# Kernel tuning notes

Measured on AMD Instinct MI355X. Metric: run time of the kernel, lower is better.

Reference implementation:

```python
import jax, jax.numpy as jnp
import numpy as np

HS = 768      # hidden_size
NH = 12       # num_heads
HD = HS // NH # head_dim = 64
WS = 8        # window_size
NG = 4        # num_global_tokens
EPS = 1e-6


def _rmsnorm(x, w):
    return x * jax.lax.rsqrt(jnp.mean(x * x, axis=-1, keepdims=True) + EPS) * w


def _attn(q, k, v, scale):
    s = jnp.einsum('...qd,...kd->...qk', q, k) * scale
    return jnp.einsum('...qk,...kd->...qd', jax.nn.softmax(s, axis=-1), v)


def _heads(t):
    # (B*, S, D) -> (B*, H, S, hd)
    return t.reshape(t.shape[0], t.shape[1], NH, HD).transpose(0, 2, 1, 3)


def setup_inputs() -> dict:
    key = jax.random.key(0)
    k0, k1, k2, k3 = jax.random.split(key, 4)
    B, N = 8, 4096
    x = jax.random.normal(k0, (B, N, HS), dtype=jnp.float32)
    w_qkv = jax.random.normal(k1, (HS, 3 * HS), dtype=jnp.float32) * 0.02
    w_out = jax.random.normal(k2, (HS, HS), dtype=jnp.float32) * 0.02
    q_norm_w = jnp.ones((HD,), dtype=jnp.float32)
    k_norm_w = jnp.ones((HD,), dtype=jnp.float32)
    global_tokens = jax.random.normal(k3, (1, NG, HS), dtype=jnp.float32) * 0.02
    return {'x': x, 'w_qkv': w_qkv, 'w_out': w_out,
            'q_norm_w': q_norm_w, 'k_norm_w': k_norm_w,
            'global_tokens': global_tokens}


def reference(x, w_qkv, w_out, q_norm_w, k_norm_w, global_tokens):
    B, N, D = x.shape
    h = w = int(np.sqrt(N))
    ws = WS
    scale = HD ** -0.5
    # ---- window partition (B, N, D) -> (B*nW, ws*ws, D) ----
    pad_h = (ws - h % ws) % ws
    pad_w = (ws - w % ws) % ws
    xg = x.reshape(B, h, w, D)
    if pad_h or pad_w:
        xg = jnp.pad(xg, ((0, 0), (0, pad_h), (0, pad_w), (0, 0)))
    hp, wp = h + pad_h, w + pad_w
    xl = xg.reshape(B, hp // ws, ws, wp // ws, ws, D)
    xl = xl.transpose(0, 1, 3, 2, 4, 5).reshape(-1, ws * ws, D)
    # ---- local window attention ----
    q, k, v = jnp.split(xl @ w_qkv, 3, axis=-1)
    q, k, v = _heads(q), _heads(k), _heads(v)
    q = _rmsnorm(q, q_norm_w)
    k = _rmsnorm(k, k_norm_w)
    o = _attn(q, k, v, scale)                      # (B*nW, H, ws*ws, hd)
    o = o.transpose(0, 2, 1, 3).reshape(-1, ws * ws, D)
    # ---- window unpartition ----
    o = o.reshape(B, hp // ws, wp // ws, ws, ws, D)
    o = o.transpose(0, 1, 3, 2, 4, 5).reshape(B, hp, wp, D)[:, :h, :w].reshape(B, N, D)
    # ---- global register tokens attend over [global; all tokens] ----
    g = jnp.broadcast_to(global_tokens, (B, NG, D))
    xf = jnp.concatenate([g, x], axis=1)           # (B, NG+N, D)
    qg, kg, vg = jnp.split(xf @ w_qkv, 3, axis=-1)
    qg = _heads(qg[:, :NG])                        # (B, H, NG, hd) -- no qk_norm in global path
    ka, va = _heads(kg), _heads(vg)                # (B, H, NG+N, hd)
    og = _attn(qg, ka, va, scale).transpose(0, 2, 1, 3).reshape(B, NG, D)
    o = o + og.mean(axis=1, keepdims=True)
    return o @ w_out
```

## Files before the change

### kernel.cpp

```cpp
#include <hip/hip_runtime.h>
#include <hip/hip_bf16.h>

typedef short short8 __attribute__((ext_vector_type(8)));
typedef unsigned short ushort8 __attribute__((ext_vector_type(8)));
typedef unsigned short ushort4v __attribute__((ext_vector_type(4)));
typedef float f32x4 __attribute__((ext_vector_type(4)));
typedef unsigned short ushort;

constexpr float SCALE = 0.125f;
constexpr float EPS_RMS = 1e-6f;

#define BAR() asm volatile("s_barrier" ::: "memory")
#define WAITV(N) asm volatile("s_waitcnt vmcnt(" #N ")" ::: "memory")

__device__ __forceinline__ ushort f2bf(float f) {
  return __builtin_bit_cast(unsigned short, __float2bfloat16(f));
}
__device__ __forceinline__ float bf2f(ushort u) {
  return __bfloat162float(__builtin_bit_cast(__hip_bfloat16, u));
}
__device__ __forceinline__ void gl_lds16(const void* g, void* l) {
  __builtin_amdgcn_global_load_lds((const __attribute__((address_space(1))) void*)g,
                                   (__attribute__((address_space(3))) void*)l, 16, 0, 0);
}

__device__ __forceinline__ int nat_row(int p) {
  return (p & ~4095) | (((p >> 9) & 7) << 9) | (((p >> 3) & 7) << 6) |
         (((p >> 6) & 7) << 3) | (p & 7);
}

__global__ void k_prep(const float* __restrict__ src, int src_ld, int mode,
                       ushort* __restrict__ hi, ushort* __restrict__ lo) {
  __shared__ float tile[64][65];
  int rb = blockIdx.x, db = blockIdx.y;
  int tid = threadIdx.x;
#pragma unroll
  for (int e = 0; e < 16; ++e) {
    int idx = e * 256 + tid;
    int dd = idx >> 6, cc = idx & 63;
    int sc;
    if (mode == 0) { int h = rb / 3, p = rb % 3; sc = p * 768 + h * 64 + cc; }
    else sc = rb * 64 + cc;
    tile[dd][cc] = src[(db * 64 + dd) * src_ld + sc];
  }
  __syncthreads();
#pragma unroll
  for (int e = 0; e < 16; ++e) {
    int idx = e * 256 + tid;
    int cc = idx >> 6, dd = idx & 63;
    float f = tile[dd][cc];
    ushort h = f2bf(f);
    ushort l = f2bf(f - bf2f(h));
    int o = (rb * 64 + cc) * 768 + db * 64 + dd;
    hi[o] = h;
    lo[o] = l;
  }
}

__global__ void k_xsplit(const float* __restrict__ x,
                         ushort* __restrict__ xh, ushort* __restrict__ xl) {
  int idx = blockIdx.x * 256 + threadIdx.x;
  int p = idx / 96, seg = idx - p * 96;
  int n = nat_row(p);
  const float* src = x + n * 768 + seg * 8;
  float4 a = *(const float4*)src;
  float4 c = *(const float4*)(src + 4);
  float v[8] = {a.x, a.y, a.z, a.w, c.x, c.y, c.z, c.w};
  ushort8 hi, lo;
#pragma unroll
  for (int j = 0; j < 8; ++j) {
    ushort h = f2bf(v[j]);
    hi[j] = h;
    lo[j] = f2bf(v[j] - bf2f(h));
  }
  *(ushort8*)&xh[p * 768 + seg * 8] = hi;
  *(ushort8*)&xl[p * 768 + seg * 8] = lo;
}

__global__ void k_gqkv(const float* __restrict__ gtok,
                       const float* __restrict__ w_qkv,
                       float* __restrict__ qkv_g) {
  int idx = blockIdx.x * 256 + threadIdx.x;
  int tok = idx / 2304, c = idx - tok * 2304;
  const float* gp = gtok + tok * 768;
  float s = 0.f;
  for (int d = 0; d < 768; ++d) s += gp[d] * w_qkv[d * 2304 + c];
  qkv_g[idx] = s;
}

#define QS_OFF 0
#define KT_OFF 4352
#define VS_OFF 8704
#define SQ_OFF 13056
#define SK_OFF 13120
#define PC_OFF 13248

__global__ __launch_bounds__(256, 2) void k_fused(
    const ushort* __restrict__ xh, const ushort* __restrict__ xl,
    const ushort* __restrict__ Whi, const ushort* __restrict__ Wlo,
    const float* __restrict__ qnw, const float* __restrict__ knw,
    const float* __restrict__ qkv_g, float* __restrict__ part,
    ushort* __restrict__ o_hi, ushort* __restrict__ o_lo) {
  __shared__ __align__(16) char smem[81920];
  const int tid = threadIdx.x;
  const int lane = tid & 63;
  const int wv = tid >> 6;
  const int wm = wv >> 1, wn = wv & 1;
  const int l15 = lane & 15, kq = lane >> 4;
  const int bid = blockIdx.x;
  const int xcd = bid & 7, kk_ = bid >> 3;
  const int h = kk_ % 12;
  const int mblk = (kk_ / 12) * 8 + xcd;
  const int r0 = mblk * 128;
  const int cb0 = h * 192;

  int gAo[4], lA[4]; bool pA[4];
#pragma unroll
  for (int j = 0; j < 4; ++j) {
    int byo = (j * 256 + tid) * 16;
    pA[j] = byo >= 8192;
    int wb = byo & 8191;
    int row = wb >> 6, sl = (wb >> 4) & 3;
    int kb = sl ^ ((row >> 1) & 3);
    gAo[j] = (r0 + row) * 768 + kb * 8;
    lA[j] = byo;
  }
  int gBo[6], lB[6]; bool pB[6];
#pragma unroll
  for (int j = 0; j < 6; ++j) {
    int byo = (j * 256 + tid) * 16;
    pB[j] = byo >= 12288;
    int wb = pB[j] ? byo - 12288 : byo;
    int row = wb >> 6, sl = (wb >> 4) & 3;
    int kb = sl ^ ((row >> 1) & 3);
    gBo[j] = (cb0 + row) * 768 + kb * 8;
    lB[j] = 16384 + byo;
  }

  f32x4 acc[4][6];
#pragma unroll
  for (int i = 0; i < 4; ++i)
#pragma unroll
    for (int j = 0; j < 6; ++j) acc[i][j] = (f32x4){0.f, 0.f, 0.f, 0.f};

  auto STAGE = [&](int t, int bufi) {
    const int kk = t * 32;
    char* bb = smem + bufi * 40960;
#pragma unroll
    for (int j = 0; j < 4; ++j) {
      const ushort* Ap = pA[j] ? xl : xh;
      gl_lds16(Ap + gAo[j] + kk, bb + lA[j]);
    }
#pragma unroll
    for (int j = 0; j < 6; ++j) {
      const ushort* Bp = pB[j] ? Wlo : Whi;
      gl_lds16(Bp + gBo[j] + kk, bb + lB[j]);
    }
  };

  auto COMPUTE = [&](int bufi) {
    const char* ba = smem + bufi * 40960;
    short8 ah[4], al[4], bh[6], bl[6];
#pragma unroll
    for (int mf = 0; mf < 4; ++mf) {
      int row = wm * 64 + mf * 16 + l15;
      int so = (kq ^ ((row >> 1) & 3)) << 4;
      ah[mf] = *(const short8*)(ba + row * 64 + so);
      al[mf] = *(const short8*)(ba + 8192 + row * 64 + so);
    }
#pragma unroll
    for (int nf = 0; nf < 6; ++nf) {
      int row = wn * 96 + nf * 16 + l15;
      int so = (kq ^ ((row >> 1) & 3)) << 4;
      bh[nf] = *(const short8*)(ba + 16384 + row * 64 + so);
      bl[nf] = *(const short8*)(ba + 28672 + row * 64 + so);
    }
#pragma unroll
    for (int mf = 0; mf < 4; ++mf)
#pragma unroll
      for (int nf = 0; nf < 6; ++nf) {
        acc[mf][nf] = __builtin_amdgcn_mfma_f32_16x16x32_bf16(ah[mf], bh[nf], acc[mf][nf], 0, 0, 0);
        acc[mf][nf] = __builtin_amdgcn_mfma_f32_16x16x32_bf16(ah[mf], bl[nf], acc[mf][nf], 0, 0, 0);
        acc[mf][nf] = __builtin_amdgcn_mfma_f32_16x16x32_bf16(al[mf], bh[nf], acc[mf][nf], 0, 0, 0);
      }
  };

  STAGE(0, 0); STAGE(1, 1);
  WAITV(10); BAR();
  for (int t = 0; t < 24; ++t) {
    int cur = t & 1;
    COMPUTE(cur);
    BAR();
    if (t < 22) { STAGE(t + 2, cur); WAITV(10); }
    else { WAITV(0); }
    BAR();
  }

  const int tl = tid;
  float* gb = (float*)smem;
  for (int pass = 0; pass < 2; ++pass) {
    if (wm == pass) {
#pragma unroll
      for (int mf = 0; mf < 4; ++mf) {
#pragma unroll
        for (int nf = 0; nf < 6; ++nf) {
          int col = wn * 96 + nf * 16 + l15;
#pragma unroll
          for (int e = 0; e < 4; ++e) {
            int tok = mf * 16 + kq * 4 + e;
            float val = acc[mf][nf][e];
            if (col < 64)       gb[QS_OFF + tok * 68 + col] = val;
            else if (col < 128) gb[KT_OFF + (col - 64) * 68 + tok] = val;
            else                gb[VS_OFF + tok * 68 + (col - 128)] = val;
          }
        }
      }
    }
    __syncthreads();

    const int widx = mblk * 2 + pass;
    const int b = widx >> 6, wl = widx & 63;

    {
      int qi = tl >> 6, j = tl & 63;
      const float* qgp = qkv_g + qi * 2304 + h * 64;
      float s = 0.f;
#pragma unroll 16
      for (int d = 0; d < 64; ++d) s += qgp[d] * gb[KT_OFF + d * 68 + j];
      s *= SCALE;
      float m = s;
#pragma unroll
      for (int o = 1; o < 64; o <<= 1) m = fmaxf(m, __shfl_xor(m, o));
      float p = expf(s - m);
      float l = p;
#pragma unroll
      for (int o = 1; o < 64; o <<= 1) l += __shfl_xor(l, o);
      gb[PC_OFF + qi * 64 + j] = p;
      int pbase = ((b * 12 + h) * 64 + wl) * 272;
      if (j == 0) { part[pbase + 256 + qi] = m; part[pbase + 260 + qi] = l; }
      __syncthreads();
      float a = 0.f;
#pragma unroll 16
      for (int jj = 0; jj < 64; ++jj) a += gb[PC_OFF + qi * 64 + jj] * gb[VS_OFF + jj * 68 + j];
      part[pbase + qi * 64 + j] = a;
    }
    __syncthreads();

    if (tl < 64) {
      float ss = 0.f;
#pragma unroll
      for (int d4 = 0; d4 < 16; ++d4) {
        f32x4 v = *(const f32x4*)&gb[QS_OFF + tl * 68 + d4 * 4];
        ss += v[0] * v[0] + v[1] * v[1] + v[2] * v[2] + v[3] * v[3];
      }
      gb[SQ_OFF + tl] = 1.0f / sqrtf(ss * 0.015625f + EPS_RMS);
    } else if (tl < 128) {
      int c = tl - 64;
      float ss = 0.f;
#pragma unroll 16
      for (int d = 0; d < 64; ++d) { float t = gb[KT_OFF + d * 68 + c]; ss += t * t; }
      gb[SK_OFF + c] = 1.0f / sqrtf(ss * 0.015625f + EPS_RMS);
    }
    __syncthreads();

    {
      const int ty = tl >> 4, tx = tl & 15;
      const int r0q = ty * 4, c0k = tx * 4;
      const f32x4* qnw4 = (const f32x4*)qnw;
      const f32x4* knw4 = (const f32x4*)knw;
      const f32x4 skv = *(const f32x4*)&gb[SK_OFF + c0k];
      f32x4 X[4];
      X[0] = X[1] = X[2] = X[3] = (f32x4){0.f, 0.f, 0.f, 0.f};
#pragma unroll
      for (int d4 = 0; d4 < 16; ++d4) {
        f32x4 ww = qnw4[d4] * knw4[d4];
        f32x4 k0 = *(const f32x4*)&gb[KT_OFF + (d4 * 4 + 0) * 68 + c0k];
        f32x4 k1 = *(const f32x4*)&gb[KT_OFF + (d4 * 4 + 1) * 68 + c0k];
        f32x4 k2 = *(const f32x4*)&gb[KT_OFF + (d4 * 4 + 2) * 68 + c0k];
        f32x4 k3 = *(const f32x4*)&gb[KT_OFF + (d4 * 4 + 3) * 68 + c0k];
#pragma unroll
        for (int r = 0; r < 4; ++r) {
          f32x4 qv = *(const f32x4*)&gb[QS_OFF + (r0q + r) * 68 + d4 * 4];
          qv *= ww;
          X[r] += qv[0] * k0 + qv[1] * k1 + qv[2] * k2 + qv[3] * k3;
        }
      }
      float li[4];
#pragma unroll
      for (int r = 0; r < 4; ++r) {
        X[r] = X[r] * skv * (gb[SQ_OFF + r0q + r] * SCALE);
        float m = fmaxf(fmaxf(X[r][0], X[r][1]), fmaxf(X[r][2], X[r][3]));
#pragma unroll
        for (int o = 1; o < 16; o <<= 1) m = fmaxf(m, __shfl_xor(m, o));
#pragma unroll
        for (int cc = 0; cc < 4; ++cc) X[r][cc] = expf(X[r][cc] - m);
        float s = X[r][0] + X[r][1] + X[r][2] + X[r][3];
#pragma unroll
        for (int o = 1; o < 16; o <<= 1) s += __shfl_xor(s, o);
        li[r] = 1.0f / s;
      }
      __syncthreads();
#pragma unroll
      for (int r = 0; r < 4; ++r)
        *(f32x4*)&gb[QS_OFF + (r0q + r) * 68 + c0k] = X[r];
      __syncthreads();
      f32x4 O[4];
      O[0] = O[1] = O[2] = O[3] = (f32x4){0.f, 0.f, 0.f, 0.f};
#pragma unroll
      for (int j4 = 0; j4 < 16; ++j4) {
        f32x4 v0 = *(const f32x4*)&gb[VS_OFF + (j4 * 4 + 0) * 68 + c0k];
        f32x4 v1 = *(const f32x4*)&gb[VS_OFF + (j4 * 4 + 1) * 68 + c0k];
        f32x4 v2 = *(const f32x4*)&gb[VS_OFF + (j4 * 4 + 2) * 68 + c0k];
        f32x4 v3 = *(const f32x4*)&gb[VS_OFF + (j4 * 4 + 3) * 68 + c0k];
#pragma unroll
        for (int r = 0; r < 4; ++r) {
          f32x4 pv = *(const f32x4*)&gb[QS_OFF + (r0q + r) * 68 + j4 * 4];
          O[r] += pv[0] * v0 + pv[1] * v1 + pv[2] * v2 + pv[3] * v3;
        }
      }
#pragma unroll
      for (int r = 0; r < 4; ++r) {
        O[r] *= li[r];
        int orow = (widx * 64 + r0q + r) * 768 + h * 64 + c0k;
        ushort4v hv, lv;
#pragma unroll
        for (int cc = 0; cc < 4; ++cc) {
          float a = O[r][cc];
          ushort hh = f2bf(a);
          hv[cc] = hh;
          lv[cc] = f2bf(a - bf2f(hh));
        }
        *(ushort4v*)&o_hi[orow] = hv;
        *(ushort4v*)&o_lo[orow] = lv;
      }
    }
    __syncthreads();
  }
}

__global__ __launch_bounds__(256, 2) void k_proj8(
    const ushort* __restrict__ o_hi, const ushort* __restrict__ o_lo,
    const ushort* __restrict__ Whi, const ushort* __restrict__ Wlo,
    const float* __restrict__ g_term, float* __restrict__ out) {
  __shared__ __align__(16) char smem[81920];
  const int tid = threadIdx.x;
  const int lane = tid & 63;
  const int wv = tid >> 6;
  const int wm = wv >> 1, wn = wv & 1;
  const int l15 = lane & 15, kq = lane >> 4;
  const int bid = blockIdx.x;
  const int xcd = bid & 7, kk_ = bid >> 3;
  const int cblk = kk_ % 4;
  const int mblk = (kk_ / 4) * 8 + xcd;
  const int r0 = mblk * 128;
  const int cb0 = cblk * 192;

  int gAo[4], lA[4]; bool pA[4];
#pragma unroll
  for (int j = 0; j < 4; ++j) {
    int byo = (j * 256 + tid) * 16;
    pA[j] = byo >= 8192;
    int wb = byo & 8191;
    int row = wb >> 6, sl = (wb >> 4) & 3;
    int kb = sl ^ ((row >> 1) & 3);
    gAo[j] = (r0 + row) * 768 + kb * 8;
    lA[j] = byo;
  }
  int gBo[6], lB[6]; bool pB[6];
#pragma unroll
  for (int j = 0; j < 6; ++j) {
    int byo = (j * 256 + tid) * 16;
    pB[j] = byo >= 12288;
    int wb = pB[j] ? byo - 12288 : byo;
    int row = wb >> 6, sl = (wb >> 4) & 3;
    int kb = sl ^ ((row >> 1) & 3);
    gBo[j] = (cb0 + row) * 768 + kb * 8;
    lB[j] = 16384 + byo;
  }

  f32x4 acc[4][6];
#pragma unroll
  for (int i = 0; i < 4; ++i)
#pragma unroll
    for (int j = 0; j < 6; ++j) acc[i][j] = (f32x4){0.f, 0.f, 0.f, 0.f};

  auto STAGE = [&](int t, int bufi) {
    const int kk = t * 32;
    char* bb = smem + bufi * 40960;
#pragma unroll
    for (int j = 0; j < 4; ++j) {
      const ushort* Ap = pA[j] ? o_lo : o_hi;
      gl_lds16(Ap + gAo[j] + kk, bb + lA[j]);
    }
#pragma unroll
    for (int j = 0; j < 6; ++j) {
      const ushort* Bp = pB[j] ? Wlo : Whi;
      gl_lds16(Bp + gBo[j] + kk, bb + lB[j]);
    }
  };

  auto COMPUTE = [&](int bufi) {
    const char* ba = smem + bufi * 40960;
    short8 ah[4], al[4], bh[6], bl[6];
#pragma unroll
    for (int mf = 0; mf < 4; ++mf) {
      int row = wm * 64 + mf * 16 + l15;
      int so = (kq ^ ((row >> 1) & 3)) << 4;
      ah[mf] = *(const short8*)(ba + row * 64 + so);
      al[mf] = *(const short8*)(ba + 8192 + row * 64 + so);
    }
#pragma unroll
    for (int nf = 0; nf < 6; ++nf) {
      int row = wn * 96 + nf * 16 + l15;
      int so = (kq ^ ((row >> 1) & 3)) << 4;
      bh[nf] = *(const short8*)(ba + 16384 + row * 64 + so);
      bl[nf] = *(const short8*)(ba + 28672 + row * 64 + so);
    }
#pragma unroll
    for (int mf = 0; mf < 4; ++mf)
#pragma unroll
      for (int nf = 0; nf < 6; ++nf) {
        acc[mf][nf] = __builtin_amdgcn_mfma_f32_16x16x32_bf16(ah[mf], bh[nf], acc[mf][nf], 0, 0, 0);
        acc[mf][nf] = __builtin_amdgcn_mfma_f32_16x16x32_bf16(ah[mf], bl[nf], acc[mf][nf], 0, 0, 0);
        acc[mf][nf] = __builtin_amdgcn_mfma_f32_16x16x32_bf16(al[mf], bh[nf], acc[mf][nf], 0, 0, 0);
      }
  };

  STAGE(0, 0); STAGE(1, 1);
  WAITV(10); BAR();
  for (int t = 0; t < 24; ++t) {
    int cur = t & 1;
    COMPUTE(cur);
    BAR();
    if (t < 22) { STAGE(t + 2, cur); WAITV(10); }
    else { WAITV(0); }
    BAR();
  }

#pragma unroll
  for (int mf = 0; mf < 4; ++mf) {
    int prow0 = r0 + wm * 64 + mf * 16 + kq * 4;
#pragma unroll
    for (int nf = 0; nf < 6; ++nf) {
      int col = cb0 + wn * 96 + nf * 16 + l15;
#pragma unroll
      for (int e = 0; e < 4; ++e) {
        int p = prow0 + e;
        out[nat_row(p) * 768 + col] = acc[mf][nf][e] + g_term[(p >> 12) * 768 + col];
      }
    }
  }
}

__global__ void k_greduce(const float* __restrict__ qkv_g,
                          const float* __restrict__ part,
                          float* __restrict__ og_mean) {
  __shared__ float red[4][64];
  int bh = blockIdx.x;
  int b = bh / 12, h = bh - b * 12;
  int tid = threadIdx.x;
  int qi = tid >> 6, d = tid & 63;
  float M = -1e30f, L = 0.f, A = 0.f;
  float qd = qkv_g[qi * 2304 + h * 64 + d];
#pragma unroll
  for (int gk = 0; gk < 4; ++gk) {
    float kd = qkv_g[gk * 2304 + 768 + h * 64 + d];
    float prod = qd * kd;
#pragma unroll
    for (int o = 1; o < 64; o <<= 1) prod += __shfl_xor(prod, o);
    float s = prod * SCALE;
    float Mn = fmaxf(M, s);
    float f = expf(M - Mn), e = expf(s - Mn);
    float vd = qkv_g[gk * 2304 + 1536 + h * 64 + d];
    A = A * f + e * vd;
    L = L * f + e;
    M = Mn;
  }
  for (int p = 0; p < 64; ++p) {
    int pbase = ((b * 12 + h) * 64 + p) * 272;
    float mp = part[pbase + 256 + qi];
    float lp = part[pbase + 260 + qi];
    float ap = part[pbase + qi * 64 + d];
    float Mn = fmaxf(M, mp);
    float f = expf(M - Mn), e = expf(mp - Mn);
    A = A * f + ap * e;
    L = L * f + lp * e;
    M = Mn;
  }
  red[qi][d] = A / L;
  __syncthreads();
  if (tid < 64) {
    float s = (red[0][d] + red[1][d] + red[2][d] + red[3][d]) * 0.25f;
    og_mean[b * 768 + h * 64 + d] = s;
  }
}

__global__ void k_gterm(const float* __restrict__ og_mean,
                        const float* __restrict__ w_out,
                        float* __restrict__ g_term) {
  int idx = blockIdx.x * 256 + threadIdx.x;
  int b = idx / 768, c = idx - b * 768;
  const float* op = og_mean + b * 768;
  float s = 0.f;
  for (int d = 0; d < 768; ++d) s += op[d] * w_out[d * 768 + c];
  g_term[idx] = s;
}

extern "C" void kernel_launch(void* const* d_in, const int* in_sizes, int n_in,
                              void* d_out, int out_size, void* d_ws, size_t ws_size,
                              hipStream_t stream) {
  const float* x      = (const float*)d_in[0];
  const float* w_qkv  = (const float*)d_in[1];
  const float* w_out  = (const float*)d_in[2];
  const float* qnw    = (const float*)d_in[3];
  const float* knw    = (const float*)d_in[4];
  const float* gtok   = (const float*)d_in[5];
  float* out = (float*)d_out;

  ushort* WhiQ = (ushort*)d_ws;
  ushort* WloQ = WhiQ + 2304 * 768;
  ushort* WhiO = WloQ + 2304 * 768;
  ushort* WloO = WhiO + 768 * 768;
  ushort* o_hi = WloO + 768 * 768;
  ushort* o_lo = o_hi + 32768 * 768;
  float* qkv_g   = (float*)(o_lo + 32768 * 768);
  float* part    = qkv_g + 9216;
  float* og_mean = part + 8 * 12 * 64 * 272;
  float* g_term  = og_mean + 6144;

  ushort* xh = (ushort*)d_out;
  ushort* xl = xh + 32768 * 768;

  k_prep  <<<dim3(36, 12), 256, 0, stream>>>(w_qkv, 2304, 0, WhiQ, WloQ);
  k_prep  <<<dim3(12, 12), 256, 0, stream>>>(w_out,  768, 1, WhiO, WloO);
  k_gqkv  <<<36,    256, 0, stream>>>(gtok, w_qkv, qkv_g);
  k_xsplit<<<12288, 256, 0, stream>>>(x, xh, xl);

  k_fused <<<3072, 256, 0, stream>>>(xh, xl, WhiQ, WloQ, qnw, knw, qkv_g, part, o_hi, o_lo);

  k_greduce<<<96, 256, 0, stream>>>(qkv_g, part, og_mean);
  k_gterm  <<<24, 256, 0, stream>>>(og_mean, w_out, g_term);
  k_proj8 <<<1024, 256, 0, stream>>>(o_hi, o_lo, WhiO, WloO, g_term, out);
}
```

Measured before the change: 690.1 us.

## Halve fused kernel M-tile to one window per block, drop two-pass epilogue

Each k_fused block now handles one 64-token window instead of two (64x192 tile, 6144 blocks). This halves LDS to 64KB and the accumulator registers, so more blocks can be resident and the serial two-pass epilogue goes away. Some syncthreads are removed, the global-attention PV step is merged into the RMS phase, and qnw*knw is precomputed in LDS. It also adds s_setprio around the MFMA loops and uses fast __expf. The cost is that the W tile is reloaded twice as often per token, which adds global and L2 traffic.

```diff
diff --git a/kernel.cpp b/kernel.cpp
--- a/kernel.cpp
+++ b/kernel.cpp
@@ -94,6 +94,7 @@
 #define SQ_OFF 13056
 #define SK_OFF 13120
 #define PC_OFF 13248
+#define WW_OFF 13504
 
 __global__ __launch_bounds__(256, 2) void k_fused(
     const ushort* __restrict__ xh, const ushort* __restrict__ xl,
@@ -101,7 +102,7 @@
     const float* __restrict__ qnw, const float* __restrict__ knw,
     const float* __restrict__ qkv_g, float* __restrict__ part,
     ushort* __restrict__ o_hi, ushort* __restrict__ o_lo) {
-  __shared__ __align__(16) char smem[81920];
+  __shared__ __align__(16) char smem[65536];
   const int tid = threadIdx.x;
   const int lane = tid & 63;
   const int wv = tid >> 6;
@@ -111,15 +112,15 @@
   const int xcd = bid & 7, kk_ = bid >> 3;
   const int h = kk_ % 12;
   const int mblk = (kk_ / 12) * 8 + xcd;
-  const int r0 = mblk * 128;
+  const int r0 = mblk * 64;
   const int cb0 = h * 192;
 
-  int gAo[4], lA[4]; bool pA[4];
-#pragma unroll
-  for (int j = 0; j < 4; ++j) {
+  int gAo[2], lA[2]; bool pA[2];
+#pragma unroll
+  for (int j = 0; j < 2; ++j) {
     int byo = (j * 256 + tid) * 16;
-    pA[j] = byo >= 8192;
-    int wb = byo & 8191;
+    pA[j] = byo >= 4096;
+    int wb = byo & 4095;
     int row = wb >> 6, sl = (wb >> 4) & 3;
     int kb = sl ^ ((row >> 1) & 3);
     gAo[j] = (r0 + row) * 768 + kb * 8;
@@ -134,20 +135,20 @@
     int row = wb >> 6, sl = (wb >> 4) & 3;
     int kb = sl ^ ((row >> 1) & 3);
     gBo[j] = (cb0 + row) * 768 + kb * 8;
-    lB[j] = 16384 + byo;
-  }
-
-  f32x4 acc[4][6];
-#pragma unroll
-  for (int i = 0; i < 4; ++i)
+    lB[j] = 8192 + byo;
+  }
+
+  f32x4 acc[2][6];
+#pragma unroll
+  for (int i = 0; i < 2; ++i)
 #pragma unroll
     for (int j = 0; j < 6; ++j) acc[i][j] = (f32x4){0.f, 0.f, 0.f, 0.f};
 
   auto STAGE = [&](int t, int bufi) {
     const int kk = t * 32;
-    char* bb = smem + bufi * 40960;
-#pragma unroll
-    for (int j = 0; j < 4; ++j) {
+    char* bb = smem + bufi * 32768;
+#pragma unroll
+    for (int j = 0; j < 2; ++j) {
       const ushort* Ap = pA[j] ? xl : xh;
       gl_lds16(Ap + gAo[j] + kk, bb + lA[j]);
     }
@@ -159,93 +160,91 @@
   };
 
   auto COMPUTE = [&](int bufi) {
-    const char* ba = smem + bufi * 40960;
-    short8 ah[4], al[4], bh[6], bl[6];
-#pragma unroll
-    for (int mf = 0; mf < 4; ++mf) {
-      int row = wm * 64 + mf * 16 + l15;
+    const char* ba = smem + bufi * 32768;
+    short8 ah[2], al[2], bh[6], bl[6];
+#pragma unroll
+    for (int mf = 0; mf < 2; ++mf) {
+      int row = wm * 32 + mf * 16 + l15;
       int so = (kq ^ ((row >> 1) & 3)) << 4;
       ah[mf] = *(const short8*)(ba + row * 64 + so);
-      al[mf] = *(const short8*)(ba + 8192 + row * 64 + so);
+      al[mf] = *(const short8*)(ba + 4096 + row * 64 + so);
     }
 #pragma unroll
     for (int nf = 0; nf < 6; ++nf) {
       int row = wn * 96 + nf * 16 + l15;
       int so = (kq ^ ((row >> 1) & 3)) << 4;
-      bh[nf] = *(const short8*)(ba + 16384 + row * 64 + so);
-      bl[nf] = *(const short8*)(ba + 28672 + row * 64 + so);
-    }
-#pragma unroll
-    for (int mf = 0; mf < 4; ++mf)
+      bh[nf] = *(const short8*)(ba + 8192 + row * 64 + so);
+      bl[nf] = *(const short8*)(ba + 20480 + row * 64 + so);
+    }
+    __builtin_amdgcn_s_setprio(1);
+#pragma unroll
+    for (int mf = 0; mf < 2; ++mf)
 #pragma unroll
       for (int nf = 0; nf < 6; ++nf) {
         acc[mf][nf] = __builtin_amdgcn_mfma_f32_16x16x32_bf16(ah[mf], bh[nf], acc[mf][nf], 0, 0, 0);
         acc[mf][nf] = __builtin_amdgcn_mfma_f32_16x16x32_bf16(ah[mf], bl[nf], acc[mf][nf], 0, 0, 0);
         acc[mf][nf] = __builtin_amdgcn_mfma_f32_16x16x32_bf16(al[mf], bh[nf], acc[mf][nf], 0, 0, 0);
       }
+    __builtin_amdgcn_s_setprio(0);
   };
 
   STAGE(0, 0); STAGE(1, 1);
-  WAITV(10); BAR();
+  WAITV(8); BAR();
   for (int t = 0; t < 24; ++t) {
     int cur = t & 1;
     COMPUTE(cur);
     BAR();
-    if (t < 22) { STAGE(t + 2, cur); WAITV(10); }
+    if (t < 22) { STAGE(t + 2, cur); WAITV(8); }
     else { WAITV(0); }
     BAR();
   }
 
   const int tl = tid;
   float* gb = (float*)smem;
-  for (int pass = 0; pass < 2; ++pass) {
-    if (wm == pass) {
-#pragma unroll
-      for (int mf = 0; mf < 4; ++mf) {
-#pragma unroll
-        for (int nf = 0; nf < 6; ++nf) {
-          int col = wn * 96 + nf * 16 + l15;
-#pragma unroll
-          for (int e = 0; e < 4; ++e) {
-            int tok = mf * 16 + kq * 4 + e;
-            float val = acc[mf][nf][e];
-            if (col < 64)       gb[QS_OFF + tok * 68 + col] = val;
-            else if (col < 128) gb[KT_OFF + (col - 64) * 68 + tok] = val;
-            else                gb[VS_OFF + tok * 68 + (col - 128)] = val;
-          }
-        }
-      }
-    }
-    __syncthreads();
-
-    const int widx = mblk * 2 + pass;
-    const int b = widx >> 6, wl = widx & 63;
-
-    {
-      int qi = tl >> 6, j = tl & 63;
-      const float* qgp = qkv_g + qi * 2304 + h * 64;
-      float s = 0.f;
-#pragma unroll 16
-      for (int d = 0; d < 64; ++d) s += qgp[d] * gb[KT_OFF + d * 68 + j];
-      s *= SCALE;
-      float m = s;
-#pragma unroll
-      for (int o = 1; o < 64; o <<= 1) m = fmaxf(m, __shfl_xor(m, o));
-      float p = expf(s - m);
-      float l = p;
-#pragma unroll
-      for (int o = 1; o < 64; o <<= 1) l += __shfl_xor(l, o);
-      gb[PC_OFF + qi * 64 + j] = p;
-      int pbase = ((b * 12 + h) * 64 + wl) * 272;
-      if (j == 0) { part[pbase + 256 + qi] = m; part[pbase + 260 + qi] = l; }
-      __syncthreads();
-      float a = 0.f;
-#pragma unroll 16
-      for (int jj = 0; jj < 64; ++jj) a += gb[PC_OFF + qi * 64 + jj] * gb[VS_OFF + jj * 68 + j];
-      part[pbase + qi * 64 + j] = a;
-    }
-    __syncthreads();
-
+#pragma unroll
+  for (int mf = 0; mf < 2; ++mf) {
+#pragma unroll
+    for (int nf = 0; nf < 6; ++nf) {
+      int col = wn * 96 + nf * 16 + l15;
+#pragma unroll
+      for (int e = 0; e < 4; ++e) {
+        int tok = wm * 32 + mf * 16 + kq * 4 + e;
+        float val = acc[mf][nf][e];
+        if (col < 64)       gb[QS_OFF + tok * 68 + col] = val;
+        else if (col < 128) gb[KT_OFF + (col - 64) * 68 + tok] = val;
+        else                gb[VS_OFF + tok * 68 + (col - 128)] = val;
+      }
+    }
+  }
+  if (tl < 64) gb[WW_OFF + tl] = qnw[tl] * knw[tl];
+  __syncthreads();
+
+  const int widx = mblk;
+  const int b = widx >> 6, wl = widx & 63;
+
+  {
+    int qi = tl >> 6, j = tl & 63;
+    const f32x4* qgp4 = (const f32x4*)(qkv_g + qi * 2304 + h * 64);
+    float s = 0.f;
+#pragma unroll
+    for (int d4 = 0; d4 < 16; ++d4) {
+      f32x4 qg = qgp4[d4];
+      s += qg[0] * gb[KT_OFF + (d4 * 4 + 0) * 68 + j] +
+           qg[1] * gb[KT_OFF + (d4 * 4 + 1) * 68 + j] +
+           qg[2] * gb[KT_OFF + (d4 * 4 + 2) * 68 + j] +
+           qg[3] * gb[KT_OFF + (d4 * 4 + 3) * 68 + j];
+    }
+    s *= SCALE;
+    float m = s;
+#pragma unroll
+    for (int o = 1; o < 64; o <<= 1) m = fmaxf(m, __shfl_xor(m, o));
+    float p = __expf(s - m);
+    float l = p;
+#pragma unroll
+    for (int o = 1; o < 64; o <<= 1) l += __shfl_xor(l, o);
+    gb[PC_OFF + qi * 64 + j] = p;
+    int pbase = ((b * 12 + h) * 64 + wl) * 272;
+    if (j == 0) { part[pbase + 256 + qi] = m; part[pbase + 260 + qi] = l; }
     if (tl < 64) {
       float ss = 0.f;
 #pragma unroll
@@ -262,79 +261,85 @@
       gb[SK_OFF + c] = 1.0f / sqrtf(ss * 0.015625f + EPS_RMS);
     }
     __syncthreads();
-
-    {
-      const int ty = tl >> 4, tx = tl & 15;
-      const int r0q = ty * 4, c0k = tx * 4;
-      const f32x4* qnw4 = (const f32x4*)qnw;
-      const f32x4* knw4 = (const f32x4*)knw;
-      const f32x4 skv = *(const f32x4*)&gb[SK_OFF + c0k];
-      f32x4 X[4];
-      X[0] = X[1] = X[2] = X[3] = (f32x4){0.f, 0.f, 0.f, 0.f};
-#pragma unroll
-      for (int d4 = 0; d4 < 16; ++d4) {
-        f32x4 ww = qnw4[d4] * knw4[d4];
-        f32x4 k0 = *(const f32x4*)&gb[KT_OFF + (d4 * 4 + 0) * 68 + c0k];
-        f32x4 k1 = *(const f32x4*)&gb[KT_OFF + (d4 * 4 + 1) * 68 + c0k];
-        f32x4 k2 = *(const f32x4*)&gb[KT_OFF + (d4 * 4 + 2) * 68 + c0k];
-        f32x4 k3 = *(const f32x4*)&gb[KT_OFF + (d4 * 4 + 3) * 68 + c0k];
-#pragma unroll
-        for (int r = 0; r < 4; ++r) {
-          f32x4 qv = *(const f32x4*)&gb[QS_OFF + (r0q + r) * 68 + d4 * 4];
-          qv *= ww;
-          X[r] += qv[0] * k0 + qv[1] * k1 + qv[2] * k2 + qv[3] * k3;
-        }
-      }
-      float li[4];
+    float a = 0.f;
+#pragma unroll
+    for (int j4 = 0; j4 < 16; ++j4) {
+      f32x4 pc = *(const f32x4*)&gb[PC_OFF + qi * 64 + j4 * 4];
+      a += pc[0] * gb[VS_OFF + (j4 * 4 + 0) * 68 + j] +
+           pc[1] * gb[VS_OFF + (j4 * 4 + 1) * 68 + j] +
+           pc[2] * gb[VS_OFF + (j4 * 4 + 2) * 68 + j] +
+           pc[3] * gb[VS_OFF + (j4 * 4 + 3) * 68 + j];
+    }
+    part[pbase + qi * 64 + j] = a;
+  }
+  __syncthreads();
+
+  {
+    const int ty = tl >> 4, tx = tl & 15;
+    const int r0q = ty * 4, c0k = tx * 4;
+    const f32x4 skv = *(const f32x4*)&gb[SK_OFF + c0k];
+    f32x4 X[4];
+    X[0] = X[1] = X[2] = X[3] = (f32x4){0.f, 0.f, 0.f, 0.f};
+#pragma unroll
+    for (int d4 = 0; d4 < 16; ++d4) {
+      f32x4 ww = *(const f32x4*)&gb[WW_OFF + d4 * 4];
+      f32x4 k0 = *(const f32x4*)&gb[KT_OFF + (d4 * 4 + 0) * 68 + c0k];
+      f32x4 k1 = *(const f32x4*)&gb[KT_OFF + (d4 * 4 + 1) * 68 + c0k];
+      f32x4 k2 = *(const f32x4*)&gb[KT_OFF + (d4 * 4 + 2) * 68 + c0k];
+      f32x4 k3 = *(const f32x4*)&gb[KT_OFF + (d4 * 4 + 3) * 68 + c0k];
 #pragma unroll
       for (int r = 0; r < 4; ++r) {
-        X[r] = X[r] * skv * (gb[SQ_OFF + r0q + r] * SCALE);
-        float m = fmaxf(fmaxf(X[r][0], X[r][1]), fmaxf(X[r][2], X[r][3]));
-#pragma unroll
-        for (int o = 1; o < 16; o <<= 1) m = fmaxf(m, __shfl_xor(m, o));
-#pragma unroll
-        for (int cc = 0; cc < 4; ++cc) X[r][cc] = expf(X[r][cc] - m);
-        float s = X[r][0] + X[r][1] + X[r][2] + X[r][3];
-#pragma unroll
-        for (int o = 1; o < 16; o <<= 1) s += __shfl_xor(s, o);
-        li[r] = 1.0f / s;
-      }
-      __syncthreads();
-#pragma unroll
-      for (int r = 0; r < 4; ++r)
-        *(f32x4*)&gb[QS_OFF + (r0q + r) * 68 + c0k] = X[r];
-      __syncthreads();
-      f32x4 O[4];
-      O[0] = O[1] = O[2] = O[3] = (f32x4){0.f, 0.f, 0.f, 0.f};
-#pragma unroll
-      for (int j4 = 0; j4 < 16; ++j4) {
-        f32x4 v0 = *(const f32x4*)&gb[VS_OFF + (j4 * 4 + 0) * 68 + c0k];
-        f32x4 v1 = *(const f32x4*)&gb[VS_OFF + (j4 * 4 + 1) * 68 + c0k];
-        f32x4 v2 = *(const f32x4*)&gb[VS_OFF + (j4 * 4 + 2) * 68 + c0k];
-        f32x4 v3 = *(const f32x4*)&gb[VS_OFF + (j4 * 4 + 3) * 68 + c0k];
-#pragma unroll
-        for (int r = 0; r < 4; ++r) {
-          f32x4 pv = *(const f32x4*)&gb[QS_OFF + (r0q + r) * 68 + j4 * 4];
-          O[r] += pv[0] * v0 + pv[1] * v1 + pv[2] * v2 + pv[3] * v3;
-        }
-      }
+        f32x4 qv = *(const f32x4*)&gb[QS_OFF + (r0q + r) * 68 + d4 * 4];
+        qv *= ww;
+        X[r] += qv[0] * k0 + qv[1] * k1 + qv[2] * k2 + qv[3] * k3;
+      }
+    }
+    float li[4];
+#pragma unroll
+    for (int r = 0; r < 4; ++r) {
+      X[r] = X[r] * skv * (gb[SQ_OFF + r0q + r] * SCALE);
+      float m = fmaxf(fmaxf(X[r][0], X[r][1]), fmaxf(X[r][2], X[r][3]));
+#pragma unroll
+      for (int o = 1; o < 16; o <<= 1) m = fmaxf(m, __shfl_xor(m, o));
+#pragma unroll
+      for (int cc = 0; cc < 4; ++cc) X[r][cc] = __expf(X[r][cc] - m);
+      float s = X[r][0] + X[r][1] + X[r][2] + X[r][3];
+#pragma unroll
+      for (int o = 1; o < 16; o <<= 1) s += __shfl_xor(s, o);
+      li[r] = 1.0f / s;
+    }
+#pragma unroll
+    for (int r = 0; r < 4; ++r)
+      *(f32x4*)&gb[QS_OFF + (r0q + r) * 68 + c0k] = X[r];
+    f32x4 O[4];
+    O[0] = O[1] = O[2] = O[3] = (f32x4){0.f, 0.f, 0.f, 0.f};
+#pragma unroll
+    for (int j4 = 0; j4 < 16; ++j4) {
+      f32x4 v0 = *(const f32x4*)&gb[VS_OFF + (j4 * 4 + 0) * 68 + c0k];
+      f32x4 v1 = *(const f32x4*)&gb[VS_OFF + (j4 * 4 + 1) * 68 + c0k];
+      f32x4 v2 = *(const f32x4*)&gb[VS_OFF + (j4 * 4 + 2) * 68 + c0k];
+      f32x4 v3 = *(const f32x4*)&gb[VS_OFF + (j4 * 4 + 3) * 68 + c0k];
 #pragma unroll
       for (int r = 0; r < 4; ++r) {
-        O[r] *= li[r];
-        int orow = (widx * 64 + r0q + r) * 768 + h * 64 + c0k;
-        ushort4v hv, lv;
-#pragma unroll
-        for (int cc = 0; cc < 4; ++cc) {
-          float a = O[r][cc];
-          ushort hh = f2bf(a);
-          hv[cc] = hh;
-          lv[cc] = f2bf(a - bf2f(hh));
-        }
-        *(ushort4v*)&o_hi[orow] = hv;
-        *(ushort4v*)&o_lo[orow] = lv;
-      }
-    }
-    __syncthreads();
+        f32x4 pv = *(const f32x4*)&gb[QS_OFF + (r0q + r) * 68 + j4 * 4];
+        O[r] += pv[0] * v0 + pv[1] * v1 + pv[2] * v2 + pv[3] * v3;
+      }
+    }
+#pragma unroll
+    for (int r = 0; r < 4; ++r) {
+      O[r] *= li[r];
+      int orow = (widx * 64 + r0q + r) * 768 + h * 64 + c0k;
+      ushort4v hv, lv;
+#pragma unroll
+      for (int cc = 0; cc < 4; ++cc) {
+        float a = O[r][cc];
+        ushort hh = f2bf(a);
+        hv[cc] = hh;
+        lv[cc] = f2bf(a - bf2f(hh));
+      }
+      *(ushort4v*)&o_hi[orow] = hv;
+      *(ushort4v*)&o_lo[orow] = lv;
+    }
   }
 }
 
@@ -416,6 +421,7 @@
       bh[nf] = *(const short8*)(ba + 16384 + row * 64 + so);
       bl[nf] = *(const short8*)(ba + 28672 + row * 64 + so);
     }
+    __builtin_amdgcn_s_setprio(1);
 #pragma unroll
     for (int mf = 0; mf < 4; ++mf)
 #pragma unroll
@@ -424,6 +430,7 @@
         acc[mf][nf] = __builtin_amdgcn_mfma_f32_16x16x32_bf16(ah[mf], bl[nf], acc[mf][nf], 0, 0, 0);
         acc[mf][nf] = __builtin_amdgcn_mfma_f32_16x16x32_bf16(al[mf], bh[nf], acc[mf][nf], 0, 0, 0);
       }
+    __builtin_amdgcn_s_setprio(0);
   };
 
   STAGE(0, 0); STAGE(1, 1);
@@ -470,7 +477,7 @@
     for (int o = 1; o < 64; o <<= 1) prod += __shfl_xor(prod, o);
     float s = prod * SCALE;
     float Mn = fmaxf(M, s);
-    float f = expf(M - Mn), e = expf(s - Mn);
+    float f = __expf(M - Mn), e = __expf(s - Mn);
     float vd = qkv_g[gk * 2304 + 1536 + h * 64 + d];
     A = A * f + e * vd;
     L = L * f + e;
@@ -482,7 +489,7 @@
     float lp = part[pbase + 260 + qi];
     float ap = part[pbase + qi * 64 + d];
     float Mn = fmaxf(M, mp);
-    float f = expf(M - Mn), e = expf(mp - Mn);
+    float f = __expf(M - Mn), e = __expf(mp - Mn);
     A = A * f + ap * e;
     L = L * f + lp * e;
     M = Mn;
@@ -536,7 +543,7 @@
   k_gqkv  <<<36,    256, 0, stream>>>(gtok, w_qkv, qkv_g);
   k_xsplit<<<12288, 256, 0, stream>>>(x, xh, xl);
 
-  k_fused <<<3072, 256, 0, stream>>>(xh, xl, WhiQ, WloQ, qnw, knw, qkv_g, part, o_hi, o_lo);
+  k_fused <<<6144, 256, 0, stream>>>(xh, xl, WhiQ, WloQ, qnw, knw, qkv_g, part, o_hi, o_lo);
 
   k_greduce<<<96, 256, 0, stream>>>(qkv_g, part, og_mean);
   k_gterm  <<<24, 256, 0, stream>>>(og_mean, w_out, g_term);
```

Measured after the change: 679.5 us. Within noise of the previous version (-1.5%).
